# Performance work log

Hardware: AMD Instinct MI355X
Metric: run time of the kernel (lower is better)

Reference implementation:

```python
import jax, jax.numpy as jnp
import numpy as np

BLOCK_SIZE = 16
NVFP4_LEVELS = np.array([0.0, 0.5, 1.0, 1.5, 2.0, 3.0, 4.0, 6.0], dtype=np.float32)


def quantize_to_nvfp4(x, block_size=BLOCK_SIZE):
    """NVFP4 fake-quant: per-16-element block, scale = amax/6, round |x| to nearest level."""
    levels = jnp.asarray(NVFP4_LEVELS, dtype=x.dtype)
    orig_shape = x.shape
    xf = x.reshape(-1, block_size)                                   # [nblk, 16]
    amax = jnp.clip(jnp.max(jnp.abs(xf), axis=-1, keepdims=True), 1e-12)
    scale = amax / 6.0                                               # [nblk, 1]
    x_norm = jnp.abs(xf) / scale                                     # in [0, 6]
    idx = jnp.argmin(jnp.abs(x_norm[..., None] - levels), axis=-1)   # nearest level (first on ties, like torch)
    x_q = jnp.sign(xf) * levels[idx] * scale
    return x_q.reshape(orig_shape)


def _magnitude_mask_2_4(w):
    # keep 2 largest-|.| of every group of 4 along in_features (row-wise 2:4)
    out_f, in_f = w.shape
    a = jnp.abs(w).reshape(out_f, in_f // 4, 4)
    thr = jnp.sort(a, axis=-1)[..., 2:3]          # 2nd-largest magnitude in group
    mask = (a >= thr).reshape(out_f, in_f)
    return mask.astype(w.dtype)


def setup_inputs() -> dict:
    key = jax.random.key(0)
    k_x, k_w, k_s, k_a, k_b, k_bias = jax.random.split(key, 6)
    B, S, IN_F, OUT_F, RANK = 2, 2048, 4096, 4096, 32
    x = jax.random.normal(k_x, (B, S, IN_F), dtype=jnp.float32)
    smooth_scale = jax.random.uniform(k_s, (IN_F,), dtype=jnp.float32, minval=0.5, maxval=2.0)
    # realistic calibrated weight: 2:4 magnitude-sparse then NVFP4 fake-quantized
    w = jax.random.normal(k_w, (OUT_F, IN_F), dtype=jnp.float32) * 0.02
    w_sparse = w * _magnitude_mask_2_4(w)
    w_quantized = quantize_to_nvfp4(w_sparse)
    lora_a = jax.random.normal(k_a, (RANK, IN_F), dtype=jnp.float32) * 0.02
    lora_b = jax.random.normal(k_b, (OUT_F, RANK), dtype=jnp.float32) * 0.02
    bias = jax.random.normal(k_bias, (OUT_F,), dtype=jnp.float32)
    return {"x": x, "smooth_scale": smooth_scale, "w_quantized": w_quantized,
            "lora_a": lora_a, "lora_b": lora_b, "bias": bias}


def reference(x, smooth_scale, w_quantized, lora_a, lora_b, bias):
    # x: [B, S, IN], smooth_scale: [IN], w_quantized: [OUT, IN]
    x_smoothed = x * smooth_scale                                    # SmoothQuant activation scaling
    x_q = quantize_to_nvfp4(x_smoothed, BLOCK_SIZE)                  # block fake-quant of activations
    base_out = jnp.einsum('bsi,oi->bso', x_q, w_quantized)           # 2:4-sparse quantized matmul
    svd_out = jnp.einsum('bsr,or->bso',
                         jnp.einsum('bsi,ri->bsr', x_smoothed, lora_a), lora_b)  # low-rank correction
    return base_out + svd_out + bias
```

## Files before the change

### kernel.cpp

```cpp
#include <hip/hip_runtime.h>
#include <hip/hip_bf16.h>
#include <stdint.h>

typedef __attribute__((ext_vector_type(8))) __bf16 bf16x8;
typedef __attribute__((ext_vector_type(4))) float f32x4;

#define KP 4160

__device__ inline void async_copy16(const void* g, void* l) {
  __builtin_amdgcn_global_load_lds((const __attribute__((address_space(1))) void*)g,
                                   (__attribute__((address_space(3))) void*)l, 16, 0, 0);
}

__global__ __launch_bounds__(256) void quant_kernel(const float* __restrict__ x,
                                                    const float* __restrict__ ss,
                                                    __bf16* __restrict__ Ab) {
  int id  = blockIdx.x * 256 + threadIdx.x;
  int row = id >> 8;
  int col = (id & 255) << 4;
  const float4* xp = (const float4*)(x + ((size_t)row << 12) + col);
  const float4* sp = (const float4*)(ss + col);
  float xs[16];
#pragma unroll
  for (int i = 0; i < 4; i++) {
    float4 xv = xp[i]; float4 sv = sp[i];
    xs[4*i+0] = xv.x * sv.x; xs[4*i+1] = xv.y * sv.y;
    xs[4*i+2] = xv.z * sv.z; xs[4*i+3] = xv.w * sv.w;
  }
  float amax = 0.f;
#pragma unroll
  for (int i = 0; i < 16; i++) amax = fmaxf(amax, fabsf(xs[i]));
  amax = fmaxf(amax, 1e-12f);
  float scale = amax / 6.0f;
  bf16x8 o0, o1;
#pragma unroll
  for (int i = 0; i < 16; i++) {
    float a  = fabsf(xs[i]);
    float xn = a / scale;
    float bestd = xn;
    float lvl   = 0.f;
    const float L[7] = {0.5f, 1.f, 1.5f, 2.f, 3.f, 4.f, 6.f};
#pragma unroll
    for (int j = 0; j < 7; j++) {
      float d = fabsf(xn - L[j]);
      if (d < bestd) { bestd = d; lvl = L[j]; }
    }
    float mag = lvl * scale;
    float q = (xs[i] > 0.f) ? mag : ((xs[i] < 0.f) ? -mag : 0.f);
    if (i < 8) o0[i] = (__bf16)q; else o1[i-8] = (__bf16)q;
  }
  __bf16* dst = Ab + (size_t)row * KP + col;
  *(bf16x8*)dst = o0;
  *(bf16x8*)(dst + 8) = o1;
}

__global__ __launch_bounds__(256) void wconv_kernel(const float* __restrict__ w,
                                                    const float* __restrict__ lb,
                                                    __bf16* __restrict__ Bb) {
  int id  = blockIdx.x * 256 + threadIdx.x;
  int row = id / 520;
  int g   = id - row * 520;
  bf16x8 v;
  if (g < 512) {
    const float4* wp = (const float4*)(w + ((size_t)row << 12) + (g << 3));
    float4 a = wp[0], b = wp[1];
    v[0]=(__bf16)a.x; v[1]=(__bf16)a.y; v[2]=(__bf16)a.z; v[3]=(__bf16)a.w;
    v[4]=(__bf16)b.x; v[5]=(__bf16)b.y; v[6]=(__bf16)b.z; v[7]=(__bf16)b.w;
  } else if (g < 516) {
    const float* p = lb + (size_t)row * 32 + ((g - 512) << 3);
#pragma unroll
    for (int j = 0; j < 8; j++) v[j] = (__bf16)p[j];
  } else {
#pragma unroll
    for (int j = 0; j < 8; j++) v[j] = (__bf16)0.f;
  }
  *(bf16x8*)(Bb + (size_t)row * KP + ((size_t)g << 3)) = v;
}

__global__ __launch_bounds__(256) void lora_kernel(const float* __restrict__ x,
                                                   const float* __restrict__ ss,
                                                   const float* __restrict__ la,
                                                   __bf16* __restrict__ Ab) {
  __shared__ float red[4][16][32];
  int tid  = threadIdx.x;
  int wave = tid >> 6, lane = tid & 63;
  int lrow = lane & 15, kg = lane >> 4;
  int m0 = blockIdx.x << 4;
  f32x4 acc0 = {0.f,0.f,0.f,0.f}, acc1 = {0.f,0.f,0.f,0.f};
  const float* xrow = x + ((size_t)(m0 + lrow) << 12);
  const float* a0   = la + ((size_t)lrow << 12);
  const float* a1   = a0 + (16 << 12);
  for (int k0 = 0; k0 < 1024; k0 += 32) {
    int kk = (wave << 10) + k0 + (kg << 3);
    bf16x8 af, b0, b1;
#pragma unroll
    for (int j = 0; j < 8; j++) {
      af[j] = (__bf16)(xrow[kk + j] * ss[kk + j]);
      b0[j] = (__bf16)a0[kk + j];
      b1[j] = (__bf16)a1[kk + j];
    }
    acc0 = __builtin_amdgcn_mfma_f32_16x16x32_bf16(af, b0, acc0, 0, 0, 0);
    acc1 = __builtin_amdgcn_mfma_f32_16x16x32_bf16(af, b1, acc1, 0, 0, 0);
  }
#pragma unroll
  for (int r = 0; r < 4; r++) {
    red[wave][kg*4 + r][lrow]      = acc0[r];
    red[wave][kg*4 + r][16 + lrow] = acc1[r];
  }
  __syncthreads();
  for (int o = tid; o < 512; o += 256) {
    int rr = o >> 5, cc = o & 31;
    float s = red[0][rr][cc] + red[1][rr][cc] + red[2][rr][cc] + red[3][rr][cc];
    __bf16* dst = Ab + (size_t)(m0 + rr) * KP + 4096;
    dst[cc]      = (__bf16)s;
    dst[32 + cc] = (__bf16)0.f;
  }
}

__global__ __launch_bounds__(256) void gemm_kernel(const __bf16* __restrict__ A,
                                                   const __bf16* __restrict__ B,
                                                   const float* __restrict__ bias,
                                                   float* __restrict__ C) {
  __shared__ __bf16 As[128 * 64];
  __shared__ __bf16 Bs[128 * 64];
  int tid  = threadIdx.x;
  int wave = tid >> 6, lane = tid & 63;
  int bm = blockIdx.x >> 5, bn = blockIdx.x & 31;
  size_t m0 = (size_t)bm << 7, n0 = (size_t)bn << 7;
  int wm = wave >> 1, wn = wave & 1;
  int lrow = lane & 15, kg = lane >> 4;
  int srow = lane >> 3;
  int sk   = ((lane & 7) ^ srow) << 3;
  f32x4 acc[4][4];
#pragma unroll
  for (int r = 0; r < 4; r++)
#pragma unroll
    for (int c = 0; c < 4; c++) acc[r][c] = (f32x4){0.f,0.f,0.f,0.f};

  for (int k = 0; k < KP; k += 64) {
#pragma unroll
    for (int i = 0; i < 4; i++) {
      int chunk = (wave << 2) + i;
      int row   = (chunk << 3) + srow;
      async_copy16(A + (m0 + row) * (size_t)KP + k + sk, (void*)(As + chunk * 512));
      async_copy16(B + (n0 + row) * (size_t)KP + k + sk, (void*)(Bs + chunk * 512));
    }
    __syncthreads();
#pragma unroll
    for (int ks = 0; ks < 2; ks++) {
      bf16x8 af[4], bfr[4];
      int kx = ((ks << 6) + (kg << 4)) ^ ((lrow & 7) << 4);
#pragma unroll
      for (int r = 0; r < 4; r++) {
        int ml = (wm << 6) + (r << 4) + lrow;
        af[r]  = *(const bf16x8*)((const char*)As + ml * 128 + kx);
        int nl = (wn << 6) + (r << 4) + lrow;
        bfr[r] = *(const bf16x8*)((const char*)Bs + nl * 128 + kx);
      }
#pragma unroll
      for (int r = 0; r < 4; r++)
#pragma unroll
        for (int c = 0; c < 4; c++)
          acc[r][c] = __builtin_amdgcn_mfma_f32_16x16x32_bf16(af[r], bfr[c], acc[r][c], 0, 0, 0);
    }
    __syncthreads();
  }
#pragma unroll
  for (int c = 0; c < 4; c++) {
    int col = (int)n0 + (wn << 6) + (c << 4) + lrow;
    float bv = bias[col];
#pragma unroll
    for (int r = 0; r < 4; r++) {
      size_t rowb = m0 + (wm << 6) + (r << 4) + (kg << 2);
#pragma unroll
      for (int q = 0; q < 4; q++)
        C[(rowb + q) * 4096 + col] = acc[r][c][q] + bv;
    }
  }
}

extern "C" void kernel_launch(void* const* d_in, const int* in_sizes, int n_in,
                              void* d_out, int out_size, void* d_ws, size_t ws_size,
                              hipStream_t stream) {
  const float* x    = (const float*)d_in[0];
  const float* ss   = (const float*)d_in[1];
  const float* w    = (const float*)d_in[2];
  const float* la   = (const float*)d_in[3];
  const float* lb   = (const float*)d_in[4];
  const float* bias = (const float*)d_in[5];
  float* out = (float*)d_out;

  __bf16* Ab = (__bf16*)d_ws;
  __bf16* Bb = Ab + (size_t)4096 * KP;

  quant_kernel<<<4096, 256, 0, stream>>>(x, ss, Ab);
  wconv_kernel<<<8320, 256, 0, stream>>>(w, lb, Bb);
  lora_kernel<<<256, 256, 0, stream>>>(x, ss, la, Ab);
  gemm_kernel<<<1024, 256, 0, stream>>>(Ab, Bb, bias, out);
}
```

Measured before the change: 356.5 us.

## Split LoRA down-projection over K into partial-sum blocks plus reduction kernel

The single LoRA kernel used only 256 blocks, each looping over all 4096 inputs. It is replaced by a split-K version with 8x more blocks writing fp32 partial sums to workspace, followed by a small kernel that reduces them and writes the bf16 result into the augmented A matrix. This is meant to fill the GPU during the LoRA stage, at the cost of an extra launch and a round trip of the partials through global memory. The old path remains as a fallback when the workspace is too small.

```diff
diff --git a/kernel.cpp b/kernel.cpp
--- a/kernel.cpp
+++ b/kernel.cpp
@@ -75,6 +75,59 @@
     for (int j = 0; j < 8; j++) v[j] = (__bf16)0.f;
   }
   *(bf16x8*)(Bb + (size_t)row * KP + ((size_t)g << 3)) = v;
+}
+
+__global__ __launch_bounds__(256) void lora_part_kernel(const float* __restrict__ x,
+                                                        const float* __restrict__ ss,
+                                                        const float* __restrict__ la,
+                                                        float* __restrict__ Tp) {
+  __shared__ float red[4][16][32];
+  int tid  = threadIdx.x;
+  int wave = tid >> 6, lane = tid & 63;
+  int lrow = lane & 15, kg = lane >> 4;
+  int m0 = blockIdx.x << 4;
+  int kbase = (blockIdx.y << 9) + (wave << 7);
+  f32x4 acc0 = {0.f,0.f,0.f,0.f}, acc1 = {0.f,0.f,0.f,0.f};
+  const float* xrow = x + ((size_t)(m0 + lrow) << 12);
+  const float* a0   = la + ((size_t)lrow << 12);
+  const float* a1   = a0 + (16 << 12);
+#pragma unroll
+  for (int k0 = 0; k0 < 128; k0 += 32) {
+    int kk = kbase + k0 + (kg << 3);
+    bf16x8 af, b0, b1;
+#pragma unroll
+    for (int j = 0; j < 8; j++) {
+      af[j] = (__bf16)(xrow[kk + j] * ss[kk + j]);
+      b0[j] = (__bf16)a0[kk + j];
+      b1[j] = (__bf16)a1[kk + j];
+    }
+    acc0 = __builtin_amdgcn_mfma_f32_16x16x32_bf16(af, b0, acc0, 0, 0, 0);
+    acc1 = __builtin_amdgcn_mfma_f32_16x16x32_bf16(af, b1, acc1, 0, 0, 0);
+  }
+#pragma unroll
+  for (int r = 0; r < 4; r++) {
+    red[wave][kg*4 + r][lrow]      = acc0[r];
+    red[wave][kg*4 + r][16 + lrow] = acc1[r];
+  }
+  __syncthreads();
+  for (int o = tid; o < 512; o += 256) {
+    int rr = o >> 5, cc = o & 31;
+    float s = red[0][rr][cc] + red[1][rr][cc] + red[2][rr][cc] + red[3][rr][cc];
+    Tp[((size_t)blockIdx.y * 4096 + m0 + rr) * 32 + cc] = s;
+  }
+}
+
+__global__ __launch_bounds__(256) void lora_fix_kernel(const float* __restrict__ Tp,
+                                                       __bf16* __restrict__ Ab) {
+  int id  = blockIdx.x * 256 + threadIdx.x;
+  int row = id >> 5, cc = id & 31;
+  float s = 0.f;
+#pragma unroll
+  for (int kc = 0; kc < 8; kc++)
+    s += Tp[((size_t)kc * 4096 + row) * 32 + cc];
+  __bf16* dst = Ab + (size_t)row * KP + 4096;
+  dst[cc]      = (__bf16)s;
+  dst[32 + cc] = (__bf16)0.f;
 }
 
 __global__ __launch_bounds__(256) void lora_kernel(const float* __restrict__ x,
@@ -192,9 +245,16 @@
 
   __bf16* Ab = (__bf16*)d_ws;
   __bf16* Bb = Ab + (size_t)4096 * KP;
+  float*  Tp = (float*)(Bb + (size_t)4096 * KP);
+  const size_t need = (size_t)2 * 4096 * KP * 2 + (size_t)8 * 4096 * 32 * 4;
 
   quant_kernel<<<4096, 256, 0, stream>>>(x, ss, Ab);
   wconv_kernel<<<8320, 256, 0, stream>>>(w, lb, Bb);
-  lora_kernel<<<256, 256, 0, stream>>>(x, ss, la, Ab);
+  if (ws_size >= need) {
+    lora_part_kernel<<<dim3(256, 8), 256, 0, stream>>>(x, ss, la, Tp);
+    lora_fix_kernel<<<512, 256, 0, stream>>>(Tp, Ab);
+  } else {
+    lora_kernel<<<256, 256, 0, stream>>>(x, ss, la, Ab);
+  }
   gemm_kernel<<<1024, 256, 0, stream>>>(Ab, Bb, bias, out);
 }
```

Result: no change. 358.1 us (+0.4%).

## Split LoRA down-projection over K into partial sums with a reduction pass

Applied to the files above, without the earlier changes.

The LoRA x·Aᵀ kernel ran only 256 blocks, each looping over 1024 K elements per wave with scalar loads. It now launches a 256x8 grid in which each block covers a 512-wide K slice, uses float4 vector loads, and writes fp32 partial sums into scratch space that aliases the weight buffer. A second small kernel adds the 8 partials and writes bf16 results into the padded columns of the A matrix. This spreads the work across far more blocks at the cost of one extra launch and a partial-sum round trip through global memory, and the scratch is overwritten later by wconv, so the kernel order now matters.

```diff
diff --git a/kernel.cpp b/kernel.cpp
--- a/kernel.cpp
+++ b/kernel.cpp
@@ -77,27 +77,38 @@
   *(bf16x8*)(Bb + (size_t)row * KP + ((size_t)g << 3)) = v;
 }
 
-__global__ __launch_bounds__(256) void lora_kernel(const float* __restrict__ x,
-                                                   const float* __restrict__ ss,
-                                                   const float* __restrict__ la,
-                                                   __bf16* __restrict__ Ab) {
+__global__ __launch_bounds__(256) void lora_part_kernel(const float* __restrict__ x,
+                                                        const float* __restrict__ ss,
+                                                        const float* __restrict__ la,
+                                                        float* __restrict__ Tp) {
   __shared__ float red[4][16][32];
   int tid  = threadIdx.x;
   int wave = tid >> 6, lane = tid & 63;
   int lrow = lane & 15, kg = lane >> 4;
   int m0 = blockIdx.x << 4;
+  int kbase = (blockIdx.y << 9) + (wave << 7);
   f32x4 acc0 = {0.f,0.f,0.f,0.f}, acc1 = {0.f,0.f,0.f,0.f};
   const float* xrow = x + ((size_t)(m0 + lrow) << 12);
   const float* a0   = la + ((size_t)lrow << 12);
   const float* a1   = a0 + (16 << 12);
-  for (int k0 = 0; k0 < 1024; k0 += 32) {
-    int kk = (wave << 10) + k0 + (kg << 3);
+#pragma unroll
+  for (int k0 = 0; k0 < 128; k0 += 32) {
+    int kk = kbase + k0 + (kg << 3);
+    float xv[8], sv[8], v0[8], v1[8];
+    *(float4*)&xv[0] = *(const float4*)(xrow + kk);
+    *(float4*)&xv[4] = *(const float4*)(xrow + kk + 4);
+    *(float4*)&sv[0] = *(const float4*)(ss + kk);
+    *(float4*)&sv[4] = *(const float4*)(ss + kk + 4);
+    *(float4*)&v0[0] = *(const float4*)(a0 + kk);
+    *(float4*)&v0[4] = *(const float4*)(a0 + kk + 4);
+    *(float4*)&v1[0] = *(const float4*)(a1 + kk);
+    *(float4*)&v1[4] = *(const float4*)(a1 + kk + 4);
     bf16x8 af, b0, b1;
 #pragma unroll
     for (int j = 0; j < 8; j++) {
-      af[j] = (__bf16)(xrow[kk + j] * ss[kk + j]);
-      b0[j] = (__bf16)a0[kk + j];
-      b1[j] = (__bf16)a1[kk + j];
+      af[j] = (__bf16)(xv[j] * sv[j]);
+      b0[j] = (__bf16)v0[j];
+      b1[j] = (__bf16)v1[j];
     }
     acc0 = __builtin_amdgcn_mfma_f32_16x16x32_bf16(af, b0, acc0, 0, 0, 0);
     acc1 = __builtin_amdgcn_mfma_f32_16x16x32_bf16(af, b1, acc1, 0, 0, 0);
@@ -111,10 +122,21 @@
   for (int o = tid; o < 512; o += 256) {
     int rr = o >> 5, cc = o & 31;
     float s = red[0][rr][cc] + red[1][rr][cc] + red[2][rr][cc] + red[3][rr][cc];
-    __bf16* dst = Ab + (size_t)(m0 + rr) * KP + 4096;
-    dst[cc]      = (__bf16)s;
-    dst[32 + cc] = (__bf16)0.f;
-  }
+    Tp[((size_t)blockIdx.y * 4096 + m0 + rr) * 32 + cc] = s;
+  }
+}
+
+__global__ __launch_bounds__(256) void lora_fix_kernel(const float* __restrict__ Tp,
+                                                       __bf16* __restrict__ Ab) {
+  int id  = blockIdx.x * 256 + threadIdx.x;
+  int row = id >> 5, cc = id & 31;
+  float s = 0.f;
+#pragma unroll
+  for (int kc = 0; kc < 8; kc++)
+    s += Tp[((size_t)kc * 4096 + row) * 32 + cc];
+  __bf16* dst = Ab + (size_t)row * KP + 4096;
+  dst[cc]      = (__bf16)s;
+  dst[32 + cc] = (__bf16)0.f;
 }
 
 __global__ __launch_bounds__(256) void gemm_kernel(const __bf16* __restrict__ A,
@@ -192,9 +214,11 @@
 
   __bf16* Ab = (__bf16*)d_ws;
   __bf16* Bb = Ab + (size_t)4096 * KP;
-
+  float* Tp = (float*)Bb;
+
+  lora_part_kernel<<<dim3(256, 8), 256, 0, stream>>>(x, ss, la, Tp);
+  lora_fix_kernel<<<512, 256, 0, stream>>>(Tp, Ab);
   quant_kernel<<<4096, 256, 0, stream>>>(x, ss, Ab);
   wconv_kernel<<<8320, 256, 0, stream>>>(w, lb, Bb);
-  lora_kernel<<<256, 256, 0, stream>>>(x, ss, la, Ab);
   gemm_kernel<<<1024, 256, 0, stream>>>(Ab, Bb, bias, out);
 }
```

Result: no change. 356.4 us (-0.0%).
